# Performance work log

Hardware: AMD Instinct MI355X
Metric: run time of the kernel (lower is better)

The kernel has to match this reference:

```python
import jax, jax.numpy as jnp
import numpy as np

B, C, H, W, O, K = 4, 64, 128, 128, 64, 3


def setup_inputs() -> dict:
    key = jax.random.key(0)
    kx, ko, kw = jax.random.split(key, 3)
    x = jax.random.normal(kx, (B, C, H, W), dtype=jnp.float32)
    offset = jax.random.normal(ko, (B, 2 * K * K, H, W), dtype=jnp.float32)
    stdv = 1.0 / np.sqrt(C * K * K)
    weight = jax.random.uniform(kw, (O, C, K, K), dtype=jnp.float32,
                                minval=-stdv, maxval=stdv)
    return {"x": x, "offset": offset, "weight": weight}


def _deform_conv(x, offset, weight):
    b, c, h, w = x.shape
    o = weight.shape[0]
    k = weight.shape[2]
    kk = k * k
    # kernel tap displacements, flattened row-major (ki*K + kj), centered at 0
    taps = jnp.arange(k) - k // 2
    di = jnp.repeat(taps, k)            # [kk]
    dj = jnp.tile(taps, k)              # [kk]
    # base sampling coords: base_i[h,1,kk], base_j[1,w,kk]
    base_i = (jnp.arange(h)[:, None, None] + di).astype(jnp.float32)
    base_j = (jnp.arange(w)[None, :, None] + dj).astype(jnp.float32)
    # offset: [b, kk, 2, h, w] -> [b, h, w, kk, 2]
    off = offset.reshape(b, kk, 2, h, w).transpose(0, 3, 4, 1, 2)
    ci = off[..., 0] + base_i           # [b,h,w,kk] float sample row coords
    cj = off[..., 1] + base_j           # [b,h,w,kk] float sample col coords

    i_lt = jnp.floor(ci).astype(jnp.int32)
    i_rb = jnp.ceil(ci).astype(jnp.int32)
    j_lt = jnp.floor(cj).astype(jnp.int32)
    j_rb = jnp.ceil(cj).astype(jnp.int32)

    def gather(ii, jj):
        # out-of-bounds samples contribute 0 (matching the torch masking)
        inb = (ii >= 0) & (ii < h) & (jj >= 0) & (jj < w)
        ic = jnp.clip(ii, 0, h - 1)
        jc = jnp.clip(jj, 0, w - 1)
        # per-image gather: xb[:, i, j] with i,j of shape [h,w,kk] -> [c,h,w,kk]
        v = jax.vmap(lambda xb, i, j: xb[:, i, j])(x, ic, jc)  # [b,c,h,w,kk]
        return v * inb[:, None].astype(x.dtype)

    vals_lt = gather(i_lt, j_lt)
    vals_rb = gather(i_rb, j_rb)
    vals_rt = gather(i_lt, j_rb)
    vals_lb = gather(i_rb, j_lt)

    # fractional parts (gradient flows to offset only through these)
    fi = (ci - i_lt.astype(ci.dtype))[:, None]   # [b,1,h,w,kk]
    fj = (cj - j_lt.astype(cj.dtype))[:, None]

    vals_t = vals_lt + fj * (vals_rt - vals_lt)
    vals_b = vals_lb + fj * (vals_rb - vals_lb)
    mapped = vals_t + fi * (vals_b - vals_t)     # [b,c,h,w,kk]

    # final GEMM: weight [o, c*kk] x im2col-like [c*kk, b*h*w]
    return jnp.einsum('ock,bchwk->bohw', weight.reshape(o, c, kk), mapped)


def reference(x, offset, weight):
    return _deform_conv(x, offset, weight)
```

## Files before the change

kernel.cpp:

```cpp
#include <hip/hip_runtime.h>

namespace {
constexpr int B = 4, C = 64, H = 128, W = 128, O = 64, KK = 9;
constexpr int PREPT = 256;
constexpr int WF_ELEMS = KK * 2 * 4 * 64 * 8;
constexpr size_t XT_BYTES = (size_t)B * H * W * C * 2;
constexpr size_t WF_BYTES = (size_t)WF_ELEMS * 2;
constexpr size_t WS_NEED  = XT_BYTES + WF_BYTES;
}

typedef float    f32x4 __attribute__((ext_vector_type(4)));
typedef _Float16 f16x2 __attribute__((ext_vector_type(2)));
typedef _Float16 f16x8 __attribute__((ext_vector_type(8)));

__device__ __forceinline__ unsigned hpack2(float a, float b) {
  f16x2 v; v[0] = (_Float16)a; v[1] = (_Float16)b;
  return __builtin_bit_cast(unsigned, v);
}
__device__ __forceinline__ void gload16(const void* g, void* l) {
  __builtin_amdgcn_global_load_lds(
      (const __attribute__((address_space(1))) unsigned*)g,
      (__attribute__((address_space(3))) unsigned*)l, 16, 0, 0);
}

__global__ __launch_bounds__(PREPT)
void prep_fused(const float* __restrict__ x, const float* __restrict__ wgt,
                unsigned* __restrict__ xt_u32, unsigned short* __restrict__ wf) {
  __shared__ float st[64][65];
  const int t = threadIdx.x;

  const int gid = blockIdx.x * PREPT + t;
  if (gid < WF_ELEMS) {
    const int e = gid & 7, lane = (gid >> 3) & 63, mt = (gid >> 9) & 3;
    const int ks = (gid >> 11) & 1, tap = gid >> 12;
    const int o = mt * 16 + (lane & 15);
    const int c = ks * 32 + ((lane >> 4) << 3) + e;
    const _Float16 hv = (_Float16)wgt[(size_t)o * (C * KK) + c * KK + tap];
    wf[gid] = __builtin_bit_cast(unsigned short, hv);
  }

  const int half = blockIdx.x & 1, h = (blockIdx.x >> 1) & 127, b = blockIdx.x >> 8;
  const int w0 = half * 64;
#pragma unroll
  for (int it = 0; it < 16; ++it) {
    const int w = t & 63, c = it * 4 + (t >> 6);
    st[w][c] = x[((size_t)(b * C + c) * H + h) * W + w0 + w];
  }
  __syncthreads();
#pragma unroll
  for (int it = 0; it < 8; ++it) {
    const int idx = it * PREPT + t;
    const int w = idx >> 5, c2 = (idx & 31) * 2;
    xt_u32[(size_t)(((b * H + h) * W) + w0 + w) * 32 + (c2 >> 1)] = hpack2(st[w][c2], st[w][c2 + 1]);
  }
}

__global__ __launch_bounds__(256) __attribute__((amdgpu_waves_per_eu(4, 4)))
void deform_mfma(const float* __restrict__ offs, const char* __restrict__ xt,
                 const char* __restrict__ wfg, float* __restrict__ out) {
  __shared__ unsigned short s_wf[2][4096];
  __shared__ unsigned short s_m[64 * 64];
  __shared__ unsigned s_pw[4][KK][16][2];
  __shared__ unsigned s_pa[4][KK][16][4];

  const int t = threadIdx.x, l = t & 63, wid = t >> 6;
  const int nid  = (blockIdx.x & 7) * 128 + (blockIdx.x >> 3);
  const int half = nid & 1, h = (nid >> 1) & 127, b = nid >> 8;
  const int wbase = half * 64 + wid * 16;

#pragma unroll
  for (int it = 0; it < 3; ++it) {
    const int item = it * 64 + l;
    if (item < KK * 16) {
      const int tap = item >> 4, pix = item & 15;
      const int ki = tap / 3, kj = tap - ki * 3;
      const int w = wbase + pix;
      const float* ob = offs + ((size_t)b * (2 * KK) + 2 * tap) * (H * W) + h * W + w;
      const float oi = ob[0], oj = ob[H * W];
      const float ci = oi + (float)(h + ki - 1);
      const float cj = oj + (float)(w + kj - 1);
      const float fli = floorf(ci), flj = floorf(cj);
      const int i0 = (int)fli, j0 = (int)flj, i1 = i0 + 1, j1 = j0 + 1;
      const float fi = ci - fli, fj = cj - flj, gi = 1.f - fi, gj = 1.f - fj;
      const bool bi0 = (unsigned)i0 < (unsigned)H, bi1 = (unsigned)i1 < (unsigned)H;
      const bool bj0 = (unsigned)j0 < (unsigned)W, bj1 = (unsigned)j1 < (unsigned)W;
      const int ic0 = min(max(i0, 0), H - 1), ic1 = min(max(i1, 0), H - 1);
      const int jc0 = min(max(j0, 0), W - 1), jc1 = min(max(j1, 0), W - 1);
      const float w00 = gi * gj * (float)(bi0 && bj0);
      const float w01 = gi * fj * (float)(bi0 && bj1);
      const float w10 = fi * gj * (float)(bi1 && bj0);
      const float w11 = fi * fj * (float)(bi1 && bj1);
      s_pw[wid][tap][pix][0] = hpack2(w00, w01);
      s_pw[wid][tap][pix][1] = hpack2(w10, w11);
      s_pa[wid][tap][pix][0] = (unsigned)(((b * H + ic0) * W + jc0) << 7);
      s_pa[wid][tap][pix][1] = (unsigned)(((b * H + ic0) * W + jc1) << 7);
      s_pa[wid][tap][pix][2] = (unsigned)(((b * H + ic1) * W + jc0) << 7);
      s_pa[wid][tap][pix][3] = (unsigned)(((b * H + ic1) * W + jc1) << 7);
    }
  }

  const int pix8 = l >> 3, oct = l & 7, cb = oct << 4;

  char* smb = (char*)s_m;
  const int wb  = ((wid * 16 + pix8) << 7) + ((oct ^ pix8) << 4);
  const int rr  = wid * 16 + (l & 15);
  const int rd0 = (rr << 7) + ((((l >> 4)    ) ^ (l & 7)) << 4);
  const int rd1 = (rr << 7) + (((4 + (l >> 4)) ^ (l & 7)) << 4);

  f32x4 acc[4];
#pragma unroll
  for (int mt = 0; mt < 4; ++mt) acc[mt] = (f32x4)0.f;

  uint4 g[2][4];
#define ISSUE(TAPX, HS) do {                                                   \
    const uint4 ad = *(const uint4*)&s_pa[wid][(TAPX)][(HS) * 8 + pix8][0];    \
    g[HS][0] = *(const uint4*)(xt + ad.x + cb);                                \
    g[HS][1] = *(const uint4*)(xt + ad.y + cb);                                \
    g[HS][2] = *(const uint4*)(xt + ad.z + cb);                                \
    g[HS][3] = *(const uint4*)(xt + ad.w + cb);                                \
  } while (0)

#define LERPH(c0_, c1_, c2_, c3_) __builtin_bit_cast(unsigned, (f16x2)(        \
    __builtin_bit_cast(f16x2, c0_) * W00 + __builtin_bit_cast(f16x2, c1_) * W01 + \
    __builtin_bit_cast(f16x2, c2_) * W10 + __builtin_bit_cast(f16x2, c3_) * W11))

#define STAGE(TAPV, HS) do {                                                   \
    const uint2 pk = *(const uint2*)&s_pw[wid][(TAPV)][(HS) * 8 + pix8][0];    \
    const f16x2 pa_ = __builtin_bit_cast(f16x2, pk.x);                         \
    const f16x2 pb_ = __builtin_bit_cast(f16x2, pk.y);                         \
    const f16x2 W00 = {pa_[0], pa_[0]}, W01 = {pa_[1], pa_[1]};                \
    const f16x2 W10 = {pb_[0], pb_[0]}, W11 = {pb_[1], pb_[1]};                \
    uint4* gc = g[HS];                                                         \
    uint4 r;                                                                   \
    r.x = LERPH(gc[0].x, gc[1].x, gc[2].x, gc[3].x);                           \
    r.y = LERPH(gc[0].y, gc[1].y, gc[2].y, gc[3].y);                           \
    r.z = LERPH(gc[0].z, gc[1].z, gc[2].z, gc[3].z);                           \
    r.w = LERPH(gc[0].w, gc[1].w, gc[2].w, gc[3].w);                           \
    *(uint4*)(smb + wb + (HS) * 1024) = r;                                     \
  } while (0)

  {
    const char* src = wfg + (size_t)t * 16;
    char* dst = (char*)s_wf + t * 16;
    gload16(src, dst);
    gload16(src + 4096, dst + 4096);
  }
  ISSUE(0, 0);
  ISSUE(0, 1);

#pragma unroll 1
  for (int tap = 0; tap < KK; ++tap) {
    __syncthreads();

    if (tap + 1 < KK) {
      const char* src = wfg + (size_t)(tap + 1) * 8192 + t * 16;
      char* dst = (char*)s_wf + ((tap + 1) & 1) * 8192 + t * 16;
      gload16(src, dst);
      gload16(src + 4096, dst + 4096);
    }

    STAGE(tap, 0);
    if (tap + 1 < KK) ISSUE(tap + 1, 0);
    STAGE(tap, 1);
    if (tap + 1 < KK) ISSUE(tap + 1, 1);

    const char* wl = (const char*)s_wf + (tap & 1) * 8192;
    const f16x8 b0 = *(const f16x8*)(smb + rd0);
    const f16x8 b1 = *(const f16x8*)(smb + rd1);
#pragma unroll
    for (int mt = 0; mt < 4; ++mt) {
      const f16x8 a0 = *(const f16x8*)(wl + mt * 1024 + l * 16);
      acc[mt] = __builtin_amdgcn_mfma_f32_16x16x32_f16(a0, b0, acc[mt], 0, 0, 0);
    }
#pragma unroll
    for (int mt = 0; mt < 4; ++mt) {
      const f16x8 a1 = *(const f16x8*)(wl + 4096 + mt * 1024 + l * 16);
      acc[mt] = __builtin_amdgcn_mfma_f32_16x16x32_f16(a1, b1, acc[mt], 0, 0, 0);
    }
  }
#undef ISSUE
#undef LERPH
#undef STAGE

#pragma unroll
  for (int mt = 0; mt < 4; ++mt)
#pragma unroll
    for (int j = 0; j < 4; ++j) {
      const int o = mt * 16 + ((l >> 4) << 2) + j;
      out[((size_t)(b * O + o) * H + h) * W + wbase + (l & 15)] = acc[mt][j];
    }
}

namespace fb {
constexpr int WT = 32, CH = 16, NCHUNK = 4, KC = 144, WPAD = 68;
}
__global__ __launch_bounds__(PREPT, 2)
void deform_conv_fused(const float* __restrict__ x, const float* __restrict__ offs,
                       const float* __restrict__ wgt, float* __restrict__ out) {
  using namespace fb;
  __shared__ int   s_i0[KK][WT];
  __shared__ int   s_j0[KK][WT];
  __shared__ float s_fi[KK][WT];
  __shared__ float s_fj[KK][WT];
  __shared__ float s_w[KC][WPAD];
  __shared__ float s_m[KC][WT + 1];
  const int t = threadIdx.x;
  const int nwt = W / WT;
  const int wt = blockIdx.x % nwt, h = (blockIdx.x / nwt) % H, b = blockIdx.x / (nwt * H);
  const int w0 = wt * WT;
  for (int idx = t; idx < KK * WT; idx += PREPT) {
    const int k = idx / WT, p = idx % WT, w = w0 + p;
    const float oi = offs[(((size_t)b * (2 * KK) + 2 * k) * H + h) * W + w];
    const float oj = offs[(((size_t)b * (2 * KK) + 2 * k + 1) * H + h) * W + w];
    const float ci = oi + (float)(h + (k / 3) - 1), cj = oj + (float)(w + (k % 3) - 1);
    const float fli = floorf(ci), flj = floorf(cj);
    s_i0[k][p] = (int)fli; s_j0[k][p] = (int)flj;
    s_fi[k][p] = ci - fli; s_fj[k][p] = cj - flj;
  }
  float acc[8];
#pragma unroll
  for (int i = 0; i < 8; ++i) acc[i] = 0.f;
  const int p = t & (WT - 1), ob = (t >> 5) * 8;
  for (int cc = 0; cc < NCHUNK; ++cc) {
    const int c0 = cc * CH;
    __syncthreads();
    for (int idx = t; idx < O * KC; idx += PREPT)
      s_w[idx % KC][idx / KC] = wgt[(size_t)(idx / KC) * (C * KK) + (size_t)c0 * KK + idx % KC];
    for (int idx = t; idx < CH * KK * WT; idx += PREPT) {
      const int pp = idx & (WT - 1), rest = idx >> 5, k = rest % KK, cl = rest / KK;
      const int i0 = s_i0[k][pp], j0 = s_j0[k][pp], i1 = i0 + 1, j1 = j0 + 1;
      const float fi = s_fi[k][pp], fj = s_fj[k][pp];
      const float* xb = x + (size_t)(b * C + c0 + cl) * H * W;
      const float v00 = ((unsigned)i0 < (unsigned)H && (unsigned)j0 < (unsigned)W) ? xb[i0 * W + j0] : 0.f;
      const float v01 = ((unsigned)i0 < (unsigned)H && (unsigned)j1 < (unsigned)W) ? xb[i0 * W + j1] : 0.f;
      const float v10 = ((unsigned)i1 < (unsigned)H && (unsigned)j0 < (unsigned)W) ? xb[i1 * W + j0] : 0.f;
      const float v11 = ((unsigned)i1 < (unsigned)H && (unsigned)j1 < (unsigned)W) ? xb[i1 * W + j1] : 0.f;
      const float top = v00 + fj * (v01 - v00), bot = v10 + fj * (v11 - v10);
      s_m[cl * KK + k][pp] = top + fi * (bot - top);
    }
    __syncthreads();
#pragma unroll 4
    for (int k = 0; k < KC; ++k) {
      const float a = s_m[k][p];
      const float4 wv0 = *reinterpret_cast<const float4*>(&s_w[k][ob]);
      const float4 wv1 = *reinterpret_cast<const float4*>(&s_w[k][ob + 4]);
      acc[0] += a * wv0.x; acc[1] += a * wv0.y; acc[2] += a * wv0.z; acc[3] += a * wv0.w;
      acc[4] += a * wv1.x; acc[5] += a * wv1.y; acc[6] += a * wv1.z; acc[7] += a * wv1.w;
    }
  }
#pragma unroll
  for (int i = 0; i < 8; ++i)
    out[(((size_t)b * O + ob + i) * H + h) * W + w0 + p] = acc[i];
}

extern "C" void kernel_launch(void* const* d_in, const int* in_sizes, int n_in,
                              void* d_out, int out_size, void* d_ws, size_t ws_size,
                              hipStream_t stream) {
  const float* x    = (const float*)d_in[0];
  const float* offs = (const float*)d_in[1];
  const float* wgt  = (const float*)d_in[2];
  float* out = (float*)d_out;

  if (ws_size < WS_NEED) {
    deform_conv_fused<<<B * H * (W / 32), PREPT, 0, stream>>>(x, offs, wgt, out);
    return;
  }
  char* xt = (char*)d_ws;
  unsigned short* wf = (unsigned short*)(xt + XT_BYTES);

  prep_fused<<<B * H * 2, PREPT, 0, stream>>>(x, wgt, (unsigned*)xt, wf);
  deform_mfma<<<B * H * 2, 256, 0, stream>>>(offs, xt, (const char*)wf, out);
}
```

Measured before the change: 31.25 us.

## Gather bilinear samples directly into MFMA B-operand layout, drop LDS staging

Each lane now gathers the corner samples for the exact pixel and channel slices it needs as the MFMA B operand and interpolates them in registers. This removes the shared-memory round trip (write, swizzle, read) for the interpolated matrix. The tap loop is fully unrolled with ping-pong register buffers, so the next tap's gathers are issued before the current tap's interpolation, with a sched barrier to keep that order. The cost is twice as many in-flight 16-byte gather registers (16 uint4 per lane), which raises register pressure at the fixed 4 waves per EU.

After: 50.33 us. +61.1%, slower.

```diff
diff --git a/kernel.cpp b/kernel.cpp
--- a/kernel.cpp
+++ b/kernel.cpp
@@ -59,7 +59,6 @@
 void deform_mfma(const float* __restrict__ offs, const char* __restrict__ xt,
                  const char* __restrict__ wfg, float* __restrict__ out) {
   __shared__ unsigned short s_wf[2][4096];
-  __shared__ unsigned short s_m[64 * 64];
   __shared__ unsigned s_pw[4][KK][16][2];
   __shared__ unsigned s_pa[4][KK][16][4];
 
@@ -99,44 +98,41 @@
     }
   }
 
-  const int pix8 = l >> 3, oct = l & 7, cb = oct << 4;
-
-  char* smb = (char*)s_m;
-  const int wb  = ((wid * 16 + pix8) << 7) + ((oct ^ pix8) << 4);
-  const int rr  = wid * 16 + (l & 15);
-  const int rd0 = (rr << 7) + ((((l >> 4)    ) ^ (l & 7)) << 4);
-  const int rd1 = (rr << 7) + (((4 + (l >> 4)) ^ (l & 7)) << 4);
+  const int px   = l & 15;
+  const int cb16 = (l >> 4) << 4;
 
   f32x4 acc[4];
 #pragma unroll
   for (int mt = 0; mt < 4; ++mt) acc[mt] = (f32x4)0.f;
 
-  uint4 g[2][4];
-#define ISSUE(TAPX, HS) do {                                                   \
-    const uint4 ad = *(const uint4*)&s_pa[wid][(TAPX)][(HS) * 8 + pix8][0];    \
-    g[HS][0] = *(const uint4*)(xt + ad.x + cb);                                \
-    g[HS][1] = *(const uint4*)(xt + ad.y + cb);                                \
-    g[HS][2] = *(const uint4*)(xt + ad.z + cb);                                \
-    g[HS][3] = *(const uint4*)(xt + ad.w + cb);                                \
+  uint4 gA[8], gB[8];
+#define ISSUE(TAPX, G) do {                                                    \
+    const uint4 ad = *(const uint4*)&s_pa[wid][(TAPX)][px][0];                 \
+    G[0] = *(const uint4*)(xt + ad.x + cb16);                                  \
+    G[1] = *(const uint4*)(xt + ad.x + cb16 + 64);                             \
+    G[2] = *(const uint4*)(xt + ad.y + cb16);                                  \
+    G[3] = *(const uint4*)(xt + ad.y + cb16 + 64);                             \
+    G[4] = *(const uint4*)(xt + ad.z + cb16);                                  \
+    G[5] = *(const uint4*)(xt + ad.z + cb16 + 64);                             \
+    G[6] = *(const uint4*)(xt + ad.w + cb16);                                  \
+    G[7] = *(const uint4*)(xt + ad.w + cb16 + 64);                             \
   } while (0)
 
-#define LERPH(c0_, c1_, c2_, c3_) __builtin_bit_cast(unsigned, (f16x2)(        \
-    __builtin_bit_cast(f16x2, c0_) * W00 + __builtin_bit_cast(f16x2, c1_) * W01 + \
-    __builtin_bit_cast(f16x2, c2_) * W10 + __builtin_bit_cast(f16x2, c3_) * W11))
-
-#define STAGE(TAPV, HS) do {                                                   \
-    const uint2 pk = *(const uint2*)&s_pw[wid][(TAPV)][(HS) * 8 + pix8][0];    \
-    const f16x2 pa_ = __builtin_bit_cast(f16x2, pk.x);                         \
-    const f16x2 pb_ = __builtin_bit_cast(f16x2, pk.y);                         \
-    const f16x2 W00 = {pa_[0], pa_[0]}, W01 = {pa_[1], pa_[1]};                \
-    const f16x2 W10 = {pb_[0], pb_[0]}, W11 = {pb_[1], pb_[1]};                \
-    uint4* gc = g[HS];                                                         \
-    uint4 r;                                                                   \
-    r.x = LERPH(gc[0].x, gc[1].x, gc[2].x, gc[3].x);                           \
-    r.y = LERPH(gc[0].y, gc[1].y, gc[2].y, gc[3].y);                           \
-    r.z = LERPH(gc[0].z, gc[1].z, gc[2].z, gc[3].z);                           \
-    r.w = LERPH(gc[0].w, gc[1].w, gc[2].w, gc[3].w);                           \
-    *(uint4*)(smb + wb + (HS) * 1024) = r;                                     \
+#define LERPW(G, KS, R) do {                                                   \
+    uint4 r_;                                                                  \
+    r_.x = __builtin_bit_cast(unsigned, (f16x2)(                               \
+      __builtin_bit_cast(f16x2, G[0 + KS].x) * W00 + __builtin_bit_cast(f16x2, G[2 + KS].x) * W01 + \
+      __builtin_bit_cast(f16x2, G[4 + KS].x) * W10 + __builtin_bit_cast(f16x2, G[6 + KS].x) * W11)); \
+    r_.y = __builtin_bit_cast(unsigned, (f16x2)(                               \
+      __builtin_bit_cast(f16x2, G[0 + KS].y) * W00 + __builtin_bit_cast(f16x2, G[2 + KS].y) * W01 + \
+      __builtin_bit_cast(f16x2, G[4 + KS].y) * W10 + __builtin_bit_cast(f16x2, G[6 + KS].y) * W11)); \
+    r_.z = __builtin_bit_cast(unsigned, (f16x2)(                               \
+      __builtin_bit_cast(f16x2, G[0 + KS].z) * W00 + __builtin_bit_cast(f16x2, G[2 + KS].z) * W01 + \
+      __builtin_bit_cast(f16x2, G[4 + KS].z) * W10 + __builtin_bit_cast(f16x2, G[6 + KS].z) * W11)); \
+    r_.w = __builtin_bit_cast(unsigned, (f16x2)(                               \
+      __builtin_bit_cast(f16x2, G[0 + KS].w) * W00 + __builtin_bit_cast(f16x2, G[2 + KS].w) * W01 + \
+      __builtin_bit_cast(f16x2, G[4 + KS].w) * W10 + __builtin_bit_cast(f16x2, G[6 + KS].w) * W11)); \
+    R = __builtin_bit_cast(f16x8, r_);                                         \
   } while (0)
 
   {
@@ -145,11 +141,13 @@
     gload16(src, dst);
     gload16(src + 4096, dst + 4096);
   }
-  ISSUE(0, 0);
-  ISSUE(0, 1);
-
-#pragma unroll 1
+  ISSUE(0, gA);
+
+#pragma unroll
   for (int tap = 0; tap < KK; ++tap) {
+    uint4* gc = (tap & 1) ? gB : gA;
+    uint4* gn = (tap & 1) ? gA : gB;
+
     __syncthreads();
 
     if (tap + 1 < KK) {
@@ -157,16 +155,20 @@
       char* dst = (char*)s_wf + ((tap + 1) & 1) * 8192 + t * 16;
       gload16(src, dst);
       gload16(src + 4096, dst + 4096);
-    }
-
-    STAGE(tap, 0);
-    if (tap + 1 < KK) ISSUE(tap + 1, 0);
-    STAGE(tap, 1);
-    if (tap + 1 < KK) ISSUE(tap + 1, 1);
+      ISSUE(tap + 1, gn);
+      __builtin_amdgcn_sched_barrier(0);
+    }
+
+    const uint2 pk = *(const uint2*)&s_pw[wid][tap][px][0];
+    const f16x2 pa_ = __builtin_bit_cast(f16x2, pk.x);
+    const f16x2 pb_ = __builtin_bit_cast(f16x2, pk.y);
+    const f16x2 W00 = {pa_[0], pa_[0]}, W01 = {pa_[1], pa_[1]};
+    const f16x2 W10 = {pb_[0], pb_[0]}, W11 = {pb_[1], pb_[1]};
+    f16x8 b0, b1;
+    LERPW(gc, 0, b0);
+    LERPW(gc, 1, b1);
 
     const char* wl = (const char*)s_wf + (tap & 1) * 8192;
-    const f16x8 b0 = *(const f16x8*)(smb + rd0);
-    const f16x8 b1 = *(const f16x8*)(smb + rd1);
 #pragma unroll
     for (int mt = 0; mt < 4; ++mt) {
       const f16x8 a0 = *(const f16x8*)(wl + mt * 1024 + l * 16);
@@ -179,15 +181,14 @@
     }
   }
 #undef ISSUE
-#undef LERPH
-#undef STAGE
+#undef LERPW
 
 #pragma unroll
   for (int mt = 0; mt < 4; ++mt)
 #pragma unroll
     for (int j = 0; j < 4; ++j) {
       const int o = mt * 16 + ((l >> 4) << 2) + j;
-      out[((size_t)(b * O + o) * H + h) * W + wbase + (l & 15)] = acc[mt][j];
+      out[((size_t)(b * O + o) * H + h) * W + wbase + px] = acc[mt][j];
     }
 }
 
```
